# Kernel optimization log

Measured on AMD Instinct MI355X. Metric: run time of the kernel, lower is better.

Reference implementation:

```python
import jax, jax.numpy as jnp
import numpy as np


def binarize_det(t):
    # Torch Binarize 'det': ((t - 0.5).sign() + 1) / 2  -> values in {0, 0.5, 1}
    return (jnp.sign(t - 0.5) + 1.0) * 0.5


def setup_inputs() -> dict:
    key = jax.random.key(0)
    k1, k2, k3 = jax.random.split(key, 3)
    B = 262144
    x = jax.random.uniform(k1, (B, 1, 1, 120), dtype=jnp.float32)
    # BNNConv2d(1, 120, kernel_size=(1,120)): weight [out=120, in=1, kh=1, kw=120],
    # init uniform(0,1) per init_w
    conv_w = jax.random.uniform(k2, (120, 1, 1, 120), dtype=jnp.float32)
    # BNNLinear(120, num_classes=1): weight [1, 120], init ~N(0.5, 0.01) per init_w
    lin_w = 0.5 + 0.01 * jax.random.normal(k3, (1, 120), dtype=jnp.float32)
    return {"x": x, "conv_w": conv_w, "lin_w": lin_w}


def reference(x, conv_w, lin_w):
    B = x.shape[0]
    # Binarize input and conv weight
    xb = binarize_det(x)          # [B,1,1,120]
    wb = binarize_det(conv_w)     # [120,1,1,120]
    # conv2d with kernel (1,120) on input [B,1,1,120] collapses to a GEMM:
    # out[b,o] = sum_k xb[b,0,0,k] * wb[o,0,0,k]
    y = jnp.einsum('bk,ok->bo', xb.reshape(B, 120), wb.reshape(120, 120))  # [B,120]
    # Softsign
    s = y / (1.0 + jnp.abs(y))
    # Flatten is identity on [B,120]; BNNLinear binarizes its input and weight, no bias
    sb = binarize_det(s)
    lwb = binarize_det(lin_w)     # [num_classes,120]
    out = jnp.einsum('bk,ck->bc', sb, lwb)  # [B,num_classes]
    return out
```

## Files before the change

### kernel.cpp

```cpp
#include <hip/hip_runtime.h>

typedef float floatx4 __attribute__((ext_vector_type(4)));

__global__ __launch_bounds__(256) void bnn_fused(
    const float* __restrict__ x, const float* __restrict__ w,
    const float* __restrict__ lin_w, float* __restrict__ out, int B)
{
    __shared__ __attribute__((aligned(16))) unsigned int T[1088];

    const int tid = threadIdx.x;
    const long r  = (long)blockIdx.x * 256 + tid;
    const long rr = (r < B) ? r : (long)B - 1;

    const floatx4* xr = (const floatx4*)(x + rr * 120);
    floatx4 buf[15];
    #pragma unroll
    for (int g = 0; g < 15; ++g) buf[g] = xr[g];

    unsigned int myvl = 0u;
    if (tid < 240) {
        const int c = tid >> 1, h = tid & 1;
        const floatx4* wr = (const floatx4*)(w + c * 120 + h * 64);
        unsigned int vh[2] = {0u, 0u}, vl[2] = {0u, 0u};
        const int ng = h ? 14 : 16;
        #pragma unroll
        for (int g = 0; g < 16; ++g) {
            if (g < ng) {
                floatx4 f = wr[g];
                #pragma unroll
                for (int j = 0; j < 4; ++j) {
                    const int kl = 4 * g + j;
                    const int wd = kl >> 5, sh = kl & 31;
                    float d = 0.5f - f[j];
                    unsigned int du = __float_as_uint(d);
                    vh[wd] |= (du >> 31) << sh;
                    vl[wd] |= (du == 0u) ? (1u << sh) : 0u;
                }
            }
        }
        T[c * 4 + 2 * h]           = vh[0];
        T[c * 4 + 2 * h + 1]       = vh[1];
        T[480 + c * 4 + 2 * h]     = vl[0];
        T[480 + c * 4 + 2 * h + 1] = vl[1];
        myvl = vl[0] | vl[1];
        if (h == 0) {
            float d = 0.5f - lin_w[c];
            unsigned int du = __float_as_uint(d);
            float hlw = (du >> 31) ? 0.5f : ((du == 0u) ? 0.25f : 0.0f);
            T[960 + c] = __float_as_uint(hlw);
        }
    }
    {
        int wany = __any((int)(myvl != 0u));
        if ((tid & 63) == 0) T[1081 + (tid >> 6)] = (unsigned int)wany;
    }
    __syncthreads();

    floatx4 buf2[15];
    #pragma unroll
    for (int g = 0; g < 15; ++g) buf2[g] = xr[15 + g];

    unsigned int uh[4] = {0u,0u,0u,0u}, ul[4] = {0u,0u,0u,0u};
    #pragma unroll
    for (int g = 0; g < 15; ++g) {
        #pragma unroll
        for (int j = 0; j < 4; ++j) {
            const int k = 4 * g + j, wd = k >> 5, sh = k & 31;
            float d = 0.5f - buf[g][j];
            unsigned int du = __float_as_uint(d);
            uh[wd] |= (du >> 31) << sh;
            ul[wd] |= (du == 0u) ? (1u << sh) : 0u;
        }
    }
    #pragma unroll
    for (int g = 0; g < 15; ++g) {
        #pragma unroll
        for (int j = 0; j < 4; ++j) {
            const int k = 60 + 4 * g + j, wd = k >> 5, sh = k & 31;
            float d = 0.5f - buf2[g][j];
            unsigned int du = __float_as_uint(d);
            uh[wd] |= (du >> 31) << sh;
            ul[wd] |= (du == 0u) ? (1u << sh) : 0u;
        }
    }

    const unsigned int flagW = T[1081] | T[1082] | T[1083] | T[1084];
    const bool rare = ((ul[0] | ul[1] | ul[2] | ul[3]) != 0u) || (flagW != 0u);

    float acc = 0.0f;
    const float* hlwt = (const float*)&T[960];
    if (!__any((int)rare)) {
        #pragma unroll 4
        for (int c = 0; c < 120; ++c) {
            const uint4 v = *(const uint4*)&T[c * 4];
            int p =  __popc(v.x & uh[0]);
            p    +=  __popc(v.y & uh[1]);
            p    +=  __popc(v.z & uh[2]);
            p    +=  __popc(v.w & uh[3]);
            acc = fmaf((float)min(p, 2), hlwt[c], acc);
        }
    } else {
        #pragma unroll 2
        for (int c = 0; c < 120; ++c) {
            const uint4 a = *(const uint4*)&T[c * 4];
            const uint4 b = *(const uint4*)&T[480 + c * 4];
            int phh = __popc(a.x & uh[0]) + __popc(a.y & uh[1]) + __popc(a.z & uh[2]) + __popc(a.w & uh[3]);
            int phl = __popc(b.x & uh[0]) + __popc(b.y & uh[1]) + __popc(b.z & uh[2]) + __popc(b.w & uh[3]);
            int plh = __popc(a.x & ul[0]) + __popc(a.y & ul[1]) + __popc(a.z & ul[2]) + __popc(a.w & ul[3]);
            int pll = __popc(b.x & ul[0]) + __popc(b.y & ul[1]) + __popc(b.z & ul[2]) + __popc(b.w & ul[3]);
            int S = 4 * phh + 2 * (phl + plh) + pll;
            int t = (S >= 4 ? 1 : 0) + (S > 4 ? 1 : 0);
            acc = fmaf((float)t, hlwt[c], acc);
        }
    }
    if (r < B) out[r] = acc;
}

extern "C" void kernel_launch(void* const* d_in, const int* in_sizes, int n_in,
                              void* d_out, int out_size, void* d_ws, size_t ws_size,
                              hipStream_t stream) {
    const float* x      = (const float*)d_in[0];
    const float* conv_w = (const float*)d_in[1];
    const float* lin_w  = (const float*)d_in[2];
    float*       out    = (float*)d_out;

    const int B = in_sizes[0] / 120;
    const int blocks = (B + 255) / 256;
    bnn_fused<<<dim3(blocks), dim3(256), 0, stream>>>(x, conv_w, lin_w, out, B);
}
```

Baseline: 199.6 us.

## Precompute binarized weights in prep kernel and skip zero-weight output channels

Measured after the change: 196.4 us. About the same (-1.6%).

```diff
diff --git a/kernel.cpp b/kernel.cpp
--- a/kernel.cpp
+++ b/kernel.cpp
@@ -2,22 +2,17 @@
 
 typedef float floatx4 __attribute__((ext_vector_type(4)));
 
-__global__ __launch_bounds__(256) void bnn_fused(
-    const float* __restrict__ x, const float* __restrict__ w,
-    const float* __restrict__ lin_w, float* __restrict__ out, int B)
+
+__global__ __launch_bounds__(256) void bnn_prep(
+    const float* __restrict__ w, const float* __restrict__ lin_w,
+    unsigned int* __restrict__ ws)
 {
-    __shared__ __attribute__((aligned(16))) unsigned int T[1088];
+    __shared__ unsigned int RH[120][4];
+    __shared__ unsigned int RL[120][4];
+    __shared__ float        HW[120];
+    __shared__ unsigned int C[2][4];
 
     const int tid = threadIdx.x;
-    const long r  = (long)blockIdx.x * 256 + tid;
-    const long rr = (r < B) ? r : (long)B - 1;
-
-    const floatx4* xr = (const floatx4*)(x + rr * 120);
-    floatx4 buf[15];
-    #pragma unroll
-    for (int g = 0; g < 15; ++g) buf[g] = xr[g];
-
-    unsigned int myvl = 0u;
     if (tid < 240) {
         const int c = tid >> 1, h = tid & 1;
         const floatx4* wr = (const floatx4*)(w + c * 120 + h * 64);
@@ -29,8 +24,7 @@
                 floatx4 f = wr[g];
                 #pragma unroll
                 for (int j = 0; j < 4; ++j) {
-                    const int kl = 4 * g + j;
-                    const int wd = kl >> 5, sh = kl & 31;
+                    const int kl = 4 * g + j, wd = kl >> 5, sh = kl & 31;
                     float d = 0.5f - f[j];
                     unsigned int du = __float_as_uint(d);
                     vh[wd] |= (du >> 31) << sh;
@@ -38,79 +32,166 @@
                 }
             }
         }
-        T[c * 4 + 2 * h]           = vh[0];
-        T[c * 4 + 2 * h + 1]       = vh[1];
-        T[480 + c * 4 + 2 * h]     = vl[0];
-        T[480 + c * 4 + 2 * h + 1] = vl[1];
-        myvl = vl[0] | vl[1];
+        RH[c][2 * h] = vh[0]; RH[c][2 * h + 1] = vh[1];
+        RL[c][2 * h] = vl[0]; RL[c][2 * h + 1] = vl[1];
         if (h == 0) {
             float d = 0.5f - lin_w[c];
             unsigned int du = __float_as_uint(d);
-            float hlw = (du >> 31) ? 0.5f : ((du == 0u) ? 0.25f : 0.0f);
-            T[960 + c] = __float_as_uint(hlw);
-        }
-    }
+            HW[c] = (du >> 31) ? 0.5f : ((du == 0u) ? 0.25f : 0.0f);
+        }
+    }
+    __syncthreads();
+
+    const int lane = tid & 63, wv = tid >> 6;
+    int cls = 0;
+    unsigned int vh4[4] = {0,0,0,0}, vl4[4] = {0,0,0,0};
+    float hl = 0.f;
+    if (tid < 120) {
+        #pragma unroll
+        for (int i = 0; i < 4; ++i) { vh4[i] = RH[tid][i]; vl4[i] = RL[tid][i]; }
+        hl = HW[tid];
+        const bool hasvl = (vl4[0] | vl4[1] | vl4[2] | vl4[3]) != 0u;
+        if (hl != 0.f) cls = hasvl ? 3 : ((hl == 0.5f) ? 1 : 2);
+    }
+    unsigned long long b1 = 0, b2 = 0, b3 = 0;
+    if (wv < 2) {
+        b1 = __ballot(cls == 1); b2 = __ballot(cls == 2); b3 = __ballot(cls == 3);
+        if (lane == 0) {
+            C[wv][1] = (unsigned)__popcll(b1);
+            C[wv][2] = (unsigned)__popcll(b2);
+            C[wv][3] = (unsigned)__popcll(b3);
+        }
+    }
+    __syncthreads();
+    const int n1 = C[0][1] + C[1][1], n2 = C[0][2] + C[1][2], n3 = C[0][3] + C[1][3];
+    if (tid == 0) { ws[0] = n1; ws[1] = n2; ws[2] = n3; ws[3] = 0u; }
+    if (cls) {
+        const unsigned long long lt = (((unsigned long long)1) << lane) - 1ull;
+        uint4* V = (uint4*)(ws + 4);
+        int idx, j = 0;
+        if (cls == 1)      idx = (wv ? (int)C[0][1] : 0) + (int)__popcll(b1 & lt);
+        else if (cls == 2) idx = n1 + (wv ? (int)C[0][2] : 0) + (int)__popcll(b2 & lt);
+        else { j = (wv ? (int)C[0][3] : 0) + (int)__popcll(b3 & lt); idx = n1 + n2 + j; }
+        V[idx] = make_uint4(vh4[0], vh4[1], vh4[2], vh4[3]);
+        if (cls == 3) {
+            ((uint4*)(ws + 484))[j] = make_uint4(vl4[0], vl4[1], vl4[2], vl4[3]);
+            ((float*)ws)[964 + j] = hl;
+        }
+    }
+}
+
+__device__ __forceinline__ int popc4(uint4 v, unsigned a, unsigned b, unsigned c, unsigned d) {
+    return __popc(v.x & a) + __popc(v.y & b) + __popc(v.z & c) + __popc(v.w & d);
+}
+
+__global__ __launch_bounds__(256, 4) void bnn_main(
+    const float* __restrict__ x, const unsigned int* __restrict__ ws,
+    float* __restrict__ out, int B)
+{
+    __shared__ __attribute__((aligned(16))) unsigned int T[1088];
+    const int tid = threadIdx.x;
+    const long r  = (long)blockIdx.x * 256 + tid;
+    const long rr = (r < B) ? r : (long)B - 1;
+    const floatx4* xr = (const floatx4*)(x + rr * 120);
+
+    floatx4 bufA[15];
+    #pragma unroll
+    for (int g = 0; g < 15; ++g) bufA[g] = xr[g];
+
     {
-        int wany = __any((int)(myvl != 0u));
-        if ((tid & 63) == 0) T[1081 + (tid >> 6)] = (unsigned int)wany;
+        const uint4* g4 = (const uint4*)ws;
+        uint4* t4 = (uint4*)T;
+        t4[tid] = g4[tid];
+        if (tid < 16) t4[256 + tid] = g4[256 + tid];
+    }
+
+    floatx4 bufB[15];
+    #pragma unroll
+    for (int g = 0; g < 15; ++g) bufB[g] = xr[15 + g];
+
+    unsigned uh0 = 0, uh1 = 0, uh2 = 0, uh3 = 0, mn = 0xFFFFFFFFu;
+    #pragma unroll
+    for (int g = 0; g < 15; ++g) {
+        #pragma unroll
+        for (int j = 0; j < 4; ++j) {
+            const int k = 4 * g + j;
+            unsigned du = __float_as_uint(0.5f - bufA[g][j]);
+            mn = min(mn, du);
+            unsigned bit = du >> 31;
+            if (k < 32) uh0 |= bit << k; else uh1 |= bit << (k - 32);
+        }
     }
     __syncthreads();
-
-    floatx4 buf2[15];
-    #pragma unroll
-    for (int g = 0; g < 15; ++g) buf2[g] = xr[15 + g];
-
-    unsigned int uh[4] = {0u,0u,0u,0u}, ul[4] = {0u,0u,0u,0u};
     #pragma unroll
     for (int g = 0; g < 15; ++g) {
         #pragma unroll
         for (int j = 0; j < 4; ++j) {
-            const int k = 4 * g + j, wd = k >> 5, sh = k & 31;
-            float d = 0.5f - buf[g][j];
-            unsigned int du = __float_as_uint(d);
-            uh[wd] |= (du >> 31) << sh;
-            ul[wd] |= (du == 0u) ? (1u << sh) : 0u;
-        }
-    }
-    #pragma unroll
-    for (int g = 0; g < 15; ++g) {
-        #pragma unroll
-        for (int j = 0; j < 4; ++j) {
-            const int k = 60 + 4 * g + j, wd = k >> 5, sh = k & 31;
-            float d = 0.5f - buf2[g][j];
-            unsigned int du = __float_as_uint(d);
-            uh[wd] |= (du >> 31) << sh;
-            ul[wd] |= (du == 0u) ? (1u << sh) : 0u;
-        }
-    }
-
-    const unsigned int flagW = T[1081] | T[1082] | T[1083] | T[1084];
-    const bool rare = ((ul[0] | ul[1] | ul[2] | ul[3]) != 0u) || (flagW != 0u);
-
-    float acc = 0.0f;
-    const float* hlwt = (const float*)&T[960];
-    if (!__any((int)rare)) {
+            const int k = 60 + 4 * g + j;
+            unsigned du = __float_as_uint(0.5f - bufB[g][j]);
+            mn = min(mn, du);
+            unsigned bit = du >> 31;
+            if (k < 64)      uh1 |= bit << (k - 32);
+            else if (k < 96) uh2 |= bit << (k - 64);
+            else             uh3 |= bit << (k - 96);
+        }
+    }
+
+    const int n1 = (int)T[0], n2 = (int)T[1], n3 = (int)T[2];
+    const uint4* V  = (const uint4*)&T[4];
+    const uint4* VL = (const uint4*)&T[484];
+    const float* HL = (const float*)&T[964];
+
+    float acc;
+    if (!__any((int)(mn == 0u))) {
+        int s1 = 0;
         #pragma unroll 4
-        for (int c = 0; c < 120; ++c) {
-            const uint4 v = *(const uint4*)&T[c * 4];
-            int p =  __popc(v.x & uh[0]);
-            p    +=  __popc(v.y & uh[1]);
-            p    +=  __popc(v.z & uh[2]);
-            p    +=  __popc(v.w & uh[3]);
-            acc = fmaf((float)min(p, 2), hlwt[c], acc);
+        for (int c = 0; c < n1; ++c) {
+            int p = popc4(V[c], uh0, uh1, uh2, uh3);
+            s1 += (p < 2 ? p : 2);
+        }
+        int s2 = 0;
+        for (int c = n1; c < n1 + n2; ++c) {
+            int p = popc4(V[c], uh0, uh1, uh2, uh3);
+            s2 += (p < 2 ? p : 2);
+        }
+        acc = fmaf((float)s1, 0.5f, 0.25f * (float)s2);
+        for (int j = 0; j < n3; ++j) {
+            int p = popc4(V[n1 + n2 + j], uh0, uh1, uh2, uh3);
+            int q = popc4(VL[j], uh0, uh1, uh2, uh3);
+            int S = 4 * p + 2 * q;
+            int t = (S >= 4 ? 1 : 0) + (S > 4 ? 1 : 0);
+            acc = fmaf((float)t, HL[j], acc);
         }
     } else {
-        #pragma unroll 2
-        for (int c = 0; c < 120; ++c) {
-            const uint4 a = *(const uint4*)&T[c * 4];
-            const uint4 b = *(const uint4*)&T[480 + c * 4];
-            int phh = __popc(a.x & uh[0]) + __popc(a.y & uh[1]) + __popc(a.z & uh[2]) + __popc(a.w & uh[3]);
-            int phl = __popc(b.x & uh[0]) + __popc(b.y & uh[1]) + __popc(b.z & uh[2]) + __popc(b.w & uh[3]);
-            int plh = __popc(a.x & ul[0]) + __popc(a.y & ul[1]) + __popc(a.z & ul[2]) + __popc(a.w & ul[3]);
-            int pll = __popc(b.x & ul[0]) + __popc(b.y & ul[1]) + __popc(b.z & ul[2]) + __popc(b.w & ul[3]);
-            int S = 4 * phh + 2 * (phl + plh) + pll;
+        unsigned ul0 = 0, ul1 = 0, ul2 = 0, ul3 = 0;
+        for (int g = 0; g < 30; ++g) {
+            floatx4 f = xr[g];
+            #pragma unroll
+            for (int j = 0; j < 4; ++j) {
+                const int k = 4 * g + j;
+                unsigned du = __float_as_uint(0.5f - f[j]);
+                unsigned e = (du == 0u) ? 1u : 0u;
+                if (k < 32)      ul0 |= e << k;
+                else if (k < 64) ul1 |= e << (k - 32);
+                else if (k < 96) ul2 |= e << (k - 64);
+                else             ul3 |= e << (k - 96);
+            }
+        }
+        int s1 = 0, s2 = 0;
+        for (int c = 0; c < n1 + n2; ++c) {
+            uint4 v = V[c];
+            int S = 4 * popc4(v, uh0, uh1, uh2, uh3) + 2 * popc4(v, ul0, ul1, ul2, ul3);
             int t = (S >= 4 ? 1 : 0) + (S > 4 ? 1 : 0);
-            acc = fmaf((float)t, hlwt[c], acc);
+            if (c < n1) s1 += t; else s2 += t;
+        }
+        acc = fmaf((float)s1, 0.5f, 0.25f * (float)s2);
+        for (int j = 0; j < n3; ++j) {
+            uint4 v = V[n1 + n2 + j], l = VL[j];
+            int S = 4 * popc4(v, uh0, uh1, uh2, uh3)
+                  + 2 * (popc4(l, uh0, uh1, uh2, uh3) + popc4(v, ul0, ul1, ul2, ul3))
+                  + popc4(l, ul0, ul1, ul2, ul3);
+            int t = (S >= 4 ? 1 : 0) + (S > 4 ? 1 : 0);
+            acc = fmaf((float)t, HL[j], acc);
         }
     }
     if (r < B) out[r] = acc;
@@ -123,8 +204,11 @@
     const float* conv_w = (const float*)d_in[1];
     const float* lin_w  = (const float*)d_in[2];
     float*       out    = (float*)d_out;
+    unsigned int* ws    = (unsigned int*)d_ws;
+
+    bnn_prep<<<dim3(1), dim3(256), 0, stream>>>(conv_w, lin_w, ws);
 
     const int B = in_sizes[0] / 120;
     const int blocks = (B + 255) / 256;
-    bnn_fused<<<dim3(blocks), dim3(256), 0, stream>>>(x, conv_w, lin_w, out, B);
-}
+    bnn_main<<<dim3(blocks), dim3(256), 0, stream>>>(x, ws, out, B);
+}
```
